# Optimization experiments

Measured on AMD Instinct MI355X. Metric: run time of the kernel, lower is better.

## Reference

```python
import jax, jax.numpy as jnp
import numpy as np

N_NODES = 50000
N_EDGES = 400000
IN_CH = 109
OUT_CH = 32


def setup_inputs() -> dict:
    key = jax.random.key(0)
    ks = jax.random.split(key, 12)
    dims = [(IN_CH, 10 * OUT_CH), (10 * OUT_CH, 2 * OUT_CH), (2 * OUT_CH, OUT_CH), (2 * OUT_CH, OUT_CH)]
    inp = {
        'x': jax.random.normal(ks[0], (N_NODES, IN_CH), dtype=jnp.float32),
        'edge_index': jax.random.randint(ks[1], (2, N_EDGES), 0, N_NODES, dtype=jnp.int64) if jax.config.jax_enable_x64 else jax.random.randint(ks[1], (2, N_EDGES), 0, N_NODES, dtype=jnp.int32),
    }
    names = ['W1', 'b1', 'W2', 'b2', 'Wmu', 'bmu', 'Wls', 'bls']
    for i, (fi, fo) in enumerate(dims):
        scale = 1.0 / np.sqrt(fi)
        inp[names[2 * i]] = jax.random.uniform(ks[2 + 2 * i], (fi, fo), minval=-scale, maxval=scale, dtype=jnp.float32)
        inp[names[2 * i + 1]] = jnp.zeros((fo,), dtype=jnp.float32)
    return inp


def _gcn_conv(x, src, dst, norm, W, b, n):
    # PyG GCNConv: h = x @ W, then symmetric-normalized aggregation, then + b
    h = x @ W                                   # [N, F_out]
    msg = h[src] * norm[:, None]                # [E+N, F_out]
    out = jax.ops.segment_sum(msg, dst, num_segments=n)
    return out + b


def _norm_and_loops(edge_index, n):
    # add self loops, compute D^{-1/2}(A+I)D^{-1/2} edge weights
    loops = jnp.arange(n, dtype=edge_index.dtype)
    src = jnp.concatenate([edge_index[0], loops])
    dst = jnp.concatenate([edge_index[1], loops])
    deg = jax.ops.segment_sum(jnp.ones_like(src, dtype=jnp.float32), dst, num_segments=n)
    dinv = jnp.where(deg > 0, jax.lax.rsqrt(jnp.maximum(deg, 1.0)), 0.0)
    norm = dinv[src] * dinv[dst]
    return src, dst, norm


def reference(x, edge_index, W1, b1, W2, b2, Wmu, bmu, Wls, bls):
    n = x.shape[0]
    src, dst, norm = _norm_and_loops(edge_index, n)
    h = jax.nn.relu(_gcn_conv(x, src, dst, norm, W1, b1, n))
    h = jax.nn.relu(_gcn_conv(h, src, dst, norm, W2, b2, n))
    mu = _gcn_conv(h, src, dst, norm, Wmu, bmu, n)
    logstd = _gcn_conv(h, src, dst, norm, Wls, bls, n)
    return (mu, logstd)
```

## Files before the change

kernel.cpp:

```cpp
#include <hip/hip_runtime.h>

#define NN 50000
#define NE 400000

typedef __attribute__((ext_vector_type(8))) short short8v;
typedef __attribute__((ext_vector_type(4))) float f32x4;

__device__ __forceinline__ unsigned short f2bf_rtn(float x) {
    unsigned u = __float_as_uint(x);
    unsigned r = u + 0x7FFFu + ((u >> 16) & 1u);
    return (unsigned short)(r >> 16);
}
__device__ __forceinline__ float bf2f(unsigned short h) {
    return __uint_as_float(((unsigned)h) << 16);
}

__global__ void prep_kernel(const float* __restrict__ x,
                            const float* __restrict__ W1, const float* __restrict__ W2,
                            const float* __restrict__ Wmu, const float* __restrict__ Wls,
                            unsigned* __restrict__ xp, int* __restrict__ zero_base,
                            unsigned short* __restrict__ w1t_hi, unsigned short* __restrict__ w1t_lo,
                            unsigned short* __restrict__ w2t_hi, unsigned short* __restrict__ w2t_lo,
                            unsigned short* __restrict__ wct_hi, unsigned short* __restrict__ wct_lo) {
    int b = blockIdx.x, tid = threadIdx.x;
    if (b < 12500) {
        int idx = b * 256 + tid;
        int i = idx >> 6, c2 = (idx & 63) * 2;
        long xb = (long)i * 109;
        float v0 = (c2 < 109) ? x[xb + c2] : 0.0f;
        float v1 = (c2 + 1 < 109) ? x[xb + c2 + 1] : 0.0f;
        xp[idx] = (unsigned)f2bf_rtn(v0) | ((unsigned)f2bf_rtn(v1) << 16);
    } else if (b < 12891) {
        int i = (b - 12500) * 256 + tid;
        if (i < 100096) zero_base[i] = 0;
    } else if (b < 13051) {
        int idx = (b - 12891) * 256 + tid;
        int n = idx >> 7, k = idx & 127;
        float v = (k < 109) ? W1[(long)k * 320 + n] : 0.0f;
        unsigned short hb = f2bf_rtn(v);
        w1t_hi[idx] = hb;
        w1t_lo[idx] = f2bf_rtn(v - bf2f(hb));
    } else if (b < 13131) {
        int idx = (b - 13051) * 256 + tid;
        int n = idx / 320, k = idx - n * 320;
        float v = W2[(long)k * 64 + n];
        unsigned short hb = f2bf_rtn(v);
        w2t_hi[idx] = hb;
        w2t_lo[idx] = f2bf_rtn(v - bf2f(hb));
    } else {
        int idx = (b - 13131) * 256 + tid;
        int n = idx >> 6, k = idx & 63;
        float v = (n < 32) ? Wmu[k * 32 + n] : Wls[k * 32 + (n - 32)];
        unsigned short hb = f2bf_rtn(v);
        wct_hi[idx] = hb;
        wct_lo[idx] = f2bf_rtn(v - bf2f(hb));
    }
}

__global__ void hist_kernel(const int* __restrict__ dst, int* __restrict__ counts) {
    for (int e = blockIdx.x * blockDim.x + threadIdx.x; e < NE; e += gridDim.x * blockDim.x)
        atomicAdd(&counts[dst[e]], 1);
}

__global__ void dinv_scan1_kernel(const int* __restrict__ counts, float* __restrict__ dinv,
                                  int* __restrict__ rowstart, int* __restrict__ bsum) {
    __shared__ int tmp[256];
    int tid = threadIdx.x;
    int i = blockIdx.x * 256 + tid;
    int v = (i < NN) ? counts[i] : 0;
    if (i < NN) dinv[i] = rsqrtf((float)(v + 1));
    tmp[tid] = v;
    __syncthreads();
    for (int off = 1; off < 256; off <<= 1) {
        int t = 0;
        if (tid >= off) t = tmp[tid - off];
        __syncthreads();
        if (tid >= off) tmp[tid] += t;
        __syncthreads();
    }
    if (i < NN) rowstart[i] = tmp[tid] - v;
    if (tid == 255) bsum[blockIdx.x] = tmp[255];
}

__global__ void scan23_kernel(int* __restrict__ rowstart, const int* __restrict__ bsum) {
    __shared__ int red[4];
    int tid = threadIdx.x;
    int v = (tid < 196 && tid < (int)blockIdx.x) ? bsum[tid] : 0;
    for (int off = 32; off > 0; off >>= 1) v += __shfl_down(v, off, 64);
    if ((tid & 63) == 0) red[tid >> 6] = v;
    __syncthreads();
    int pref = red[0] + red[1] + red[2] + red[3];
    int i = blockIdx.x * 256 + tid;
    if (i < NN) rowstart[i] += pref;
    if (i == 0) rowstart[NN] = NE;
}

__global__ void scatter_kernel(const int* __restrict__ src, const int* __restrict__ dst,
                               const int* __restrict__ rowstart, int* __restrict__ cursor,
                               int* __restrict__ esrc) {
    for (int e = blockIdx.x * blockDim.x + threadIdx.x; e < NE; e += gridDim.x * blockDim.x) {
        int d = dst[e];
        int pos = rowstart[d] + atomicAdd(&cursor[d], 1);
        esrc[pos] = src[e];
    }
}

__global__ __launch_bounds__(256) void agg109_packed_kernel(const int* __restrict__ rowstart,
                                                            const int* __restrict__ esrc,
                                                            const float* __restrict__ dinv,
                                                            const unsigned* __restrict__ xp,
                                                            unsigned* __restrict__ xa_hi32) {
    int wave = blockIdx.x * (blockDim.x >> 6) + (threadIdx.x >> 6);
    if (wave >= NN) return;
    int lane = threadIdx.x & 63;
    float wd = dinv[wave];
    unsigned pself = xp[(long)wave * 64 + lane];
    float acc0 = __uint_as_float(pself << 16) * wd;
    float acc1 = __uint_as_float(pself & 0xFFFF0000u) * wd;
    int j0 = rowstart[wave], j1 = rowstart[wave + 1];
    int j = j0;
    for (; j + 8 <= j1; j += 8) {
        int s[8];
        float w[8];
        unsigned pp[8];
        #pragma unroll
        for (int u = 0; u < 8; ++u) s[u] = esrc[j + u];
        #pragma unroll
        for (int u = 0; u < 8; ++u) w[u] = dinv[s[u]];
        #pragma unroll
        for (int u = 0; u < 8; ++u) pp[u] = xp[(long)s[u] * 64 + lane];
        #pragma unroll
        for (int u = 0; u < 8; ++u) {
            acc0 = fmaf(__uint_as_float(pp[u] << 16), w[u], acc0);
            acc1 = fmaf(__uint_as_float(pp[u] & 0xFFFF0000u), w[u], acc1);
        }
    }
    for (; j + 4 <= j1; j += 4) {
        int s0 = esrc[j], s1 = esrc[j + 1], s2 = esrc[j + 2], s3 = esrc[j + 3];
        float w0 = dinv[s0], w1 = dinv[s1], w2 = dinv[s2], w3 = dinv[s3];
        unsigned p0 = xp[(long)s0 * 64 + lane], p1 = xp[(long)s1 * 64 + lane];
        unsigned p2 = xp[(long)s2 * 64 + lane], p3 = xp[(long)s3 * 64 + lane];
        acc0 = fmaf(__uint_as_float(p0 << 16), w0, acc0);
        acc1 = fmaf(__uint_as_float(p0 & 0xFFFF0000u), w0, acc1);
        acc0 = fmaf(__uint_as_float(p1 << 16), w1, acc0);
        acc1 = fmaf(__uint_as_float(p1 & 0xFFFF0000u), w1, acc1);
        acc0 = fmaf(__uint_as_float(p2 << 16), w2, acc0);
        acc1 = fmaf(__uint_as_float(p2 & 0xFFFF0000u), w2, acc1);
        acc0 = fmaf(__uint_as_float(p3 << 16), w3, acc0);
        acc1 = fmaf(__uint_as_float(p3 & 0xFFFF0000u), w3, acc1);
    }
    for (; j < j1; ++j) {
        int s = esrc[j];
        float w = dinv[s];
        unsigned pv = xp[(long)s * 64 + lane];
        acc0 = fmaf(__uint_as_float(pv << 16), w, acc0);
        acc1 = fmaf(__uint_as_float(pv & 0xFFFF0000u), w, acc1);
    }
    acc0 *= wd;
    acc1 *= wd;
    xa_hi32[(long)wave * 64 + lane] =
        (unsigned)f2bf_rtn(acc0) | ((unsigned)f2bf_rtn(acc1) << 16);
}

__global__ __launch_bounds__(256) void agg64_relu_bf16_kernel(const int* __restrict__ rowstart,
                                                              const int* __restrict__ esrc,
                                                              const float* __restrict__ dinv,
                                                              const unsigned short* __restrict__ g,
                                                              const float* __restrict__ b,
                                                              unsigned short* __restrict__ hhi) {
    int wave = blockIdx.x * (blockDim.x >> 6) + (threadIdx.x >> 6);
    if (wave >= NN) return;
    int lane = threadIdx.x & 63;
    long base = (long)wave * 64;
    float acc = bf2f(g[base + lane]);
    int j0 = rowstart[wave], j1 = rowstart[wave + 1];
    int j = j0;
    for (; j + 4 <= j1; j += 4) {
        int s0 = esrc[j], s1 = esrc[j + 1], s2 = esrc[j + 2], s3 = esrc[j + 3];
        float p0 = bf2f(g[(long)s0 * 64 + lane]), p1 = bf2f(g[(long)s1 * 64 + lane]);
        float p2 = bf2f(g[(long)s2 * 64 + lane]), p3 = bf2f(g[(long)s3 * 64 + lane]);
        acc += p0 + p1 + p2 + p3;
    }
    for (; j < j1; ++j) acc += bf2f(g[(long)esrc[j] * 64 + lane]);
    float v = acc * dinv[wave] + b[lane];
    v = v > 0.0f ? v : 0.0f;
    hhi[base + lane] = f2bf_rtn(v);
}

__global__ __launch_bounds__(256) void agg64b_kernel(const int* __restrict__ rowstart,
                                                     const int* __restrict__ esrc,
                                                     const float* __restrict__ dinv,
                                                     const unsigned short* __restrict__ h,
                                                     unsigned short* __restrict__ a_hi) {
    int wave = blockIdx.x * (blockDim.x >> 6) + (threadIdx.x >> 6);
    if (wave >= NN) return;
    int lane = threadIdx.x & 63;
    long base = (long)wave * 64;
    float wd = dinv[wave];
    float acc = bf2f(h[base + lane]) * wd;
    int j0 = rowstart[wave], j1 = rowstart[wave + 1];
    int j = j0;
    for (; j + 4 <= j1; j += 4) {
        int s0 = esrc[j], s1 = esrc[j + 1], s2 = esrc[j + 2], s3 = esrc[j + 3];
        float w0 = dinv[s0], w1 = dinv[s1], w2 = dinv[s2], w3 = dinv[s3];
        float p0 = bf2f(h[(long)s0 * 64 + lane]), p1 = bf2f(h[(long)s1 * 64 + lane]);
        float p2 = bf2f(h[(long)s2 * 64 + lane]), p3 = bf2f(h[(long)s3 * 64 + lane]);
        acc = fmaf(p0, w0, acc); acc = fmaf(p1, w1, acc);
        acc = fmaf(p2, w2, acc); acc = fmaf(p3, w3, acc);
    }
    for (; j < j1; ++j) {
        int s = esrc[j];
        acc = fmaf(bf2f(h[(long)s * 64 + lane]), dinv[s], acc);
    }
    a_hi[base + lane] = f2bf_rtn(acc * wd);
}

#define LDT 72

template <int MODE>
__global__ __launch_bounds__(256) void mfma_gemm_kernel(
    const unsigned short* __restrict__ Ahi,
    const unsigned short* __restrict__ Bhi, const unsigned short* __restrict__ Blo,
    const float* __restrict__ bias, const float* __restrict__ bias2,
    const float* __restrict__ dinv,
    unsigned short* __restrict__ Chi,
    float* __restrict__ Cf, int M, int N, int K, int grid_n) {
    __shared__ unsigned short As[64 * LDT];
    __shared__ unsigned short Bs[2 * 64 * LDT];
    int tid = threadIdx.x;
    int wid = tid >> 6, lane = tid & 63;
    int l15 = lane & 15, l4 = lane >> 4;

    int T = gridDim.x;
    int xcd = blockIdx.x & 7, jj = blockIdx.x >> 3;
    int q = T >> 3, r = T & 7;
    int start = (xcd < r) ? xcd * (q + 1) : r * (q + 1) + (xcd - r) * q;
    int lin = start + jj;
    int bm = lin / grid_n, bn = lin - bm * grid_n;
    int bm0 = bm * 64, bn0 = bn * 64;

    f32x4 acc[4] = {};

    for (int kc = 0; kc < K; kc += 64) {
        #pragma unroll
        for (int r2 = 0; r2 < 2; ++r2) {
            int idx = tid + 256 * r2;
            int row = idx >> 3, slot = idx & 7;
            int grow = bm0 + row;
            if (grow >= M) grow = M - 1;
            long go = (long)grow * K + kc + slot * 8;
            *(uint4*)&As[row * LDT + slot * 8] = *(const uint4*)&Ahi[go];
            long gob = (long)(bn0 + row) * K + kc + slot * 8;
            *(uint4*)&Bs[row * LDT + slot * 8] = *(const uint4*)&Bhi[gob];
            *(uint4*)&Bs[64 * LDT + row * LDT + slot * 8] = *(const uint4*)&Blo[gob];
        }
        __syncthreads();
        #pragma unroll
        for (int ks = 0; ks < 2; ++ks) {
            int koff = ks * 32 + l4 * 8;
            int ra = (wid * 16 + l15) * LDT + koff;
            short8v ah = *(const short8v*)&As[ra];
            #pragma unroll
            for (int n = 0; n < 4; ++n) {
                int rb = (n * 16 + l15) * LDT + koff;
                short8v bh = *(const short8v*)&Bs[rb];
                short8v bl = *(const short8v*)&Bs[64 * LDT + rb];
                acc[n] = __builtin_amdgcn_mfma_f32_16x16x32_bf16(ah, bh, acc[n], 0, 0, 0);
                acc[n] = __builtin_amdgcn_mfma_f32_16x16x32_bf16(ah, bl, acc[n], 0, 0, 0);
            }
        }
        __syncthreads();
    }
    int rbase = bm0 + wid * 16 + l4 * 4;
    #pragma unroll
    for (int q2 = 0; q2 < 4; ++q2) {
        int grow = rbase + q2;
        if (grow >= M) continue;
        float rs = (MODE == 1) ? dinv[grow] : 0.0f;
        #pragma unroll
        for (int n = 0; n < 4; ++n) {
            int gcol = bn0 + n * 16 + l15;
            float v = acc[n][q2];
            if (MODE == 0) {
                v += bias[gcol];
                v = v > 0.0f ? v : 0.0f;
                Chi[(long)grow * N + gcol] = f2bf_rtn(v);
            } else if (MODE == 1) {
                Chi[(long)grow * N + gcol] = f2bf_rtn(v * rs);
            } else {
                if (gcol < 32)
                    Cf[(long)grow * 32 + gcol] = v + bias[gcol];
                else
                    Cf[(long)NN * 32 + (long)grow * 32 + (gcol - 32)] = v + bias2[gcol - 32];
            }
        }
    }
}

extern "C" void kernel_launch(void* const* d_in, const int* in_sizes, int n_in,
                              void* d_out, int out_size, void* d_ws, size_t ws_size,
                              hipStream_t stream) {
    const float* x   = (const float*)d_in[0];
    const int*   ei  = (const int*)d_in[1];
    const int*   src = ei;
    const int*   dst = ei + NE;
    const float* W1  = (const float*)d_in[2];
    const float* b1  = (const float*)d_in[3];
    const float* W2  = (const float*)d_in[4];
    const float* b2  = (const float*)d_in[5];
    const float* Wmu = (const float*)d_in[6];
    const float* bmu = (const float*)d_in[7];
    const float* Wls = (const float*)d_in[8];
    const float* bls = (const float*)d_in[9];
    float* out = (float*)d_out;

    char* p = (char*)d_ws;
    float* dinv   = (float*)p; p += 50048 * 4;
    int* counts   = (int*)p;   p += 50048 * 4;
    int* cursor   = (int*)p;   p += 50048 * 4;
    int* rowstart = (int*)p;   p += 50056 * 4;
    int* bsum     = (int*)p;   p += 256 * 4;
    int* esrc     = (int*)p;   p += 400000 * 4;
    unsigned* xp          = (unsigned*)p;       p += 50000L * 64 * 4;
    unsigned short* xa_hi = (unsigned short*)p; p += 50000L * 128 * 2;
    unsigned short* a2_hi = (unsigned short*)p; p += 50000L * 64 * 2;
    unsigned short* g2b   = (unsigned short*)p; p += 50000L * 64 * 2;
    unsigned short* h1_hi = (unsigned short*)p; p += 50000L * 320 * 2;
    unsigned short* w1t_hi = (unsigned short*)p; p += 320 * 128 * 2;
    unsigned short* w1t_lo = (unsigned short*)p; p += 320 * 128 * 2;
    unsigned short* w2t_hi = (unsigned short*)p; p += 64 * 320 * 2;
    unsigned short* w2t_lo = (unsigned short*)p; p += 64 * 320 * 2;
    unsigned short* wct_hi = (unsigned short*)p; p += 64 * 64 * 2;
    unsigned short* wct_lo = (unsigned short*)p; p += 64 * 64 * 2;
    unsigned short* h2_hi = xa_hi;

    const int TB = 256;
    const int NB_NODES = (NN + TB - 1) / TB;
    const int NB_AGG = (NN * 64 + TB - 1) / TB;

    prep_kernel<<<13147, TB, 0, stream>>>(x, W1, W2, Wmu, Wls, xp, counts,
                                          w1t_hi, w1t_lo, w2t_hi, w2t_lo, wct_hi, wct_lo);
    hist_kernel<<<1024, TB, 0, stream>>>(dst, counts);
    dinv_scan1_kernel<<<NB_NODES, TB, 0, stream>>>(counts, dinv, rowstart, bsum);
    scan23_kernel<<<NB_NODES, TB, 0, stream>>>(rowstart, bsum);
    scatter_kernel<<<1024, TB, 0, stream>>>(src, dst, rowstart, cursor, esrc);

    agg109_packed_kernel<<<NB_AGG, TB, 0, stream>>>(rowstart, esrc, dinv, xp,
                                                    (unsigned*)xa_hi);
    mfma_gemm_kernel<0><<<782 * 5, 256, 0, stream>>>(xa_hi, w1t_hi, w1t_lo, b1,
                                                     nullptr, nullptr, h1_hi, nullptr,
                                                     NN, 320, 128, 5);

    mfma_gemm_kernel<1><<<782, 256, 0, stream>>>(h1_hi, w2t_hi, w2t_lo, nullptr,
                                                 nullptr, dinv, g2b, nullptr,
                                                 NN, 64, 320, 1);
    agg64_relu_bf16_kernel<<<NB_AGG, TB, 0, stream>>>(rowstart, esrc, dinv, g2b, b2, h2_hi);

    agg64b_kernel<<<NB_AGG, TB, 0, stream>>>(rowstart, esrc, dinv, h2_hi, a2_hi);
    mfma_gemm_kernel<3><<<782, 256, 0, stream>>>(a2_hi, wct_hi, wct_lo, bmu,
                                                 bls, nullptr, nullptr, out,
                                                 NN, 64, 64, 1);
}
```

Baseline: 183.9 us.

## Fuse CSR build into cooperative kernel and drop W1 low-part MFMA

Replaces the histogram, two scan kernels and the scatter kernel with a single cooperative-launch kernel that uses grid-wide syncs, and moves the zeroing of counts and cursor into it. This removes several kernel launches and the gaps between them. It also drops the bf16 low-part correction for W1 in the first GEMM, halving its MFMA count and B-tile loads at the cost of reduced weight precision in layer one.

```diff
diff --git a/kernel.cpp b/kernel.cpp
--- a/kernel.cpp
+++ b/kernel.cpp
@@ -1,7 +1,10 @@
 #include <hip/hip_runtime.h>
+#include <hip/hip_cooperative_groups.h>
 
 #define NN 50000
 #define NE 400000
+
+namespace cg = cooperative_groups;
 
 typedef __attribute__((ext_vector_type(8))) short short8v;
 typedef __attribute__((ext_vector_type(4))) float f32x4;
@@ -18,8 +21,8 @@
 __global__ void prep_kernel(const float* __restrict__ x,
                             const float* __restrict__ W1, const float* __restrict__ W2,
                             const float* __restrict__ Wmu, const float* __restrict__ Wls,
-                            unsigned* __restrict__ xp, int* __restrict__ zero_base,
-                            unsigned short* __restrict__ w1t_hi, unsigned short* __restrict__ w1t_lo,
+                            unsigned* __restrict__ xp,
+                            unsigned short* __restrict__ w1t_hi,
                             unsigned short* __restrict__ w2t_hi, unsigned short* __restrict__ w2t_lo,
                             unsigned short* __restrict__ wct_hi, unsigned short* __restrict__ wct_lo) {
     int b = blockIdx.x, tid = threadIdx.x;
@@ -30,25 +33,20 @@
         float v0 = (c2 < 109) ? x[xb + c2] : 0.0f;
         float v1 = (c2 + 1 < 109) ? x[xb + c2 + 1] : 0.0f;
         xp[idx] = (unsigned)f2bf_rtn(v0) | ((unsigned)f2bf_rtn(v1) << 16);
-    } else if (b < 12891) {
-        int i = (b - 12500) * 256 + tid;
-        if (i < 100096) zero_base[i] = 0;
-    } else if (b < 13051) {
-        int idx = (b - 12891) * 256 + tid;
+    } else if (b < 12660) {
+        int idx = (b - 12500) * 256 + tid;
         int n = idx >> 7, k = idx & 127;
         float v = (k < 109) ? W1[(long)k * 320 + n] : 0.0f;
-        unsigned short hb = f2bf_rtn(v);
-        w1t_hi[idx] = hb;
-        w1t_lo[idx] = f2bf_rtn(v - bf2f(hb));
-    } else if (b < 13131) {
-        int idx = (b - 13051) * 256 + tid;
+        w1t_hi[idx] = f2bf_rtn(v);
+    } else if (b < 12740) {
+        int idx = (b - 12660) * 256 + tid;
         int n = idx / 320, k = idx - n * 320;
         float v = W2[(long)k * 64 + n];
         unsigned short hb = f2bf_rtn(v);
         w2t_hi[idx] = hb;
         w2t_lo[idx] = f2bf_rtn(v - bf2f(hb));
     } else {
-        int idx = (b - 13131) * 256 + tid;
+        int idx = (b - 12740) * 256 + tid;
         int n = idx >> 6, k = idx & 63;
         float v = (n < 32) ? Wmu[k * 32 + n] : Wls[k * 32 + (n - 32)];
         unsigned short hb = f2bf_rtn(v);
@@ -57,48 +55,49 @@
     }
 }
 
-__global__ void hist_kernel(const int* __restrict__ dst, int* __restrict__ counts) {
-    for (int e = blockIdx.x * blockDim.x + threadIdx.x; e < NE; e += gridDim.x * blockDim.x)
-        atomicAdd(&counts[dst[e]], 1);
-}
-
-__global__ void dinv_scan1_kernel(const int* __restrict__ counts, float* __restrict__ dinv,
-                                  int* __restrict__ rowstart, int* __restrict__ bsum) {
+__global__ void csr_build_kernel(const int* __restrict__ src, const int* __restrict__ dst,
+                                 int* __restrict__ counts, int* __restrict__ cursor,
+                                 float* __restrict__ dinv, int* __restrict__ rowstart,
+                                 int* __restrict__ bsum, int* __restrict__ esrc) {
+    cg::grid_group grid = cg::this_grid();
     __shared__ int tmp[256];
-    int tid = threadIdx.x;
-    int i = blockIdx.x * 256 + tid;
-    int v = (i < NN) ? counts[i] : 0;
-    if (i < NN) dinv[i] = rsqrtf((float)(v + 1));
-    tmp[tid] = v;
-    __syncthreads();
-    for (int off = 1; off < 256; off <<= 1) {
-        int t = 0;
-        if (tid >= off) t = tmp[tid - off];
+    __shared__ int red[4];
+    int tid = threadIdx.x, b = blockIdx.x;
+    int gid = b * 256 + tid, gsz = gridDim.x * 256;
+
+    for (int i = gid; i < NN; i += gsz) { counts[i] = 0; cursor[i] = 0; }
+    grid.sync();
+    for (int e = gid; e < NE; e += gsz) atomicAdd(&counts[dst[e]], 1);
+    grid.sync();
+    if (b < 196) {
+        int i = gid;
+        int v = (i < NN) ? counts[i] : 0;
+        if (i < NN) dinv[i] = rsqrtf((float)(v + 1));
+        tmp[tid] = v;
         __syncthreads();
-        if (tid >= off) tmp[tid] += t;
+        for (int off = 1; off < 256; off <<= 1) {
+            int t = 0;
+            if (tid >= off) t = tmp[tid - off];
+            __syncthreads();
+            if (tid >= off) tmp[tid] += t;
+            __syncthreads();
+        }
+        if (i < NN) rowstart[i] = tmp[tid] - v;
+        if (tid == 255) bsum[b] = tmp[255];
+    }
+    grid.sync();
+    if (b < 196) {
+        int v = (tid < 196 && tid < b) ? bsum[tid] : 0;
+        for (int off = 32; off > 0; off >>= 1) v += __shfl_down(v, off, 64);
+        if ((tid & 63) == 0) red[tid >> 6] = v;
         __syncthreads();
-    }
-    if (i < NN) rowstart[i] = tmp[tid] - v;
-    if (tid == 255) bsum[blockIdx.x] = tmp[255];
-}
-
-__global__ void scan23_kernel(int* __restrict__ rowstart, const int* __restrict__ bsum) {
-    __shared__ int red[4];
-    int tid = threadIdx.x;
-    int v = (tid < 196 && tid < (int)blockIdx.x) ? bsum[tid] : 0;
-    for (int off = 32; off > 0; off >>= 1) v += __shfl_down(v, off, 64);
-    if ((tid & 63) == 0) red[tid >> 6] = v;
-    __syncthreads();
-    int pref = red[0] + red[1] + red[2] + red[3];
-    int i = blockIdx.x * 256 + tid;
-    if (i < NN) rowstart[i] += pref;
-    if (i == 0) rowstart[NN] = NE;
-}
-
-__global__ void scatter_kernel(const int* __restrict__ src, const int* __restrict__ dst,
-                               const int* __restrict__ rowstart, int* __restrict__ cursor,
-                               int* __restrict__ esrc) {
-    for (int e = blockIdx.x * blockDim.x + threadIdx.x; e < NE; e += gridDim.x * blockDim.x) {
+        int pref = red[0] + red[1] + red[2] + red[3];
+        int i = gid;
+        if (i < NN) rowstart[i] += pref;
+        if (i == 0) rowstart[NN] = NE;
+    }
+    grid.sync();
+    for (int e = gid; e < NE; e += gsz) {
         int d = dst[e];
         int pos = rowstart[d] + atomicAdd(&cursor[d], 1);
         esrc[pos] = src[e];
@@ -225,8 +224,9 @@
     const float* __restrict__ dinv,
     unsigned short* __restrict__ Chi,
     float* __restrict__ Cf, int M, int N, int K, int grid_n) {
+    constexpr bool BLO = (MODE != 0);
     __shared__ unsigned short As[64 * LDT];
-    __shared__ unsigned short Bs[2 * 64 * LDT];
+    __shared__ unsigned short Bs[(BLO ? 2 : 1) * 64 * LDT];
     int tid = threadIdx.x;
     int wid = tid >> 6, lane = tid & 63;
     int l15 = lane & 15, l4 = lane >> 4;
@@ -252,7 +252,7 @@
             *(uint4*)&As[row * LDT + slot * 8] = *(const uint4*)&Ahi[go];
             long gob = (long)(bn0 + row) * K + kc + slot * 8;
             *(uint4*)&Bs[row * LDT + slot * 8] = *(const uint4*)&Bhi[gob];
-            *(uint4*)&Bs[64 * LDT + row * LDT + slot * 8] = *(const uint4*)&Blo[gob];
+            if (BLO) *(uint4*)&Bs[64 * LDT + row * LDT + slot * 8] = *(const uint4*)&Blo[gob];
         }
         __syncthreads();
         #pragma unroll
@@ -264,9 +264,11 @@
             for (int n = 0; n < 4; ++n) {
                 int rb = (n * 16 + l15) * LDT + koff;
                 short8v bh = *(const short8v*)&Bs[rb];
-                short8v bl = *(const short8v*)&Bs[64 * LDT + rb];
                 acc[n] = __builtin_amdgcn_mfma_f32_16x16x32_bf16(ah, bh, acc[n], 0, 0, 0);
-                acc[n] = __builtin_amdgcn_mfma_f32_16x16x32_bf16(ah, bl, acc[n], 0, 0, 0);
+                if (BLO) {
+                    short8v bl = *(const short8v*)&Bs[64 * LDT + rb];
+                    acc[n] = __builtin_amdgcn_mfma_f32_16x16x32_bf16(ah, bl, acc[n], 0, 0, 0);
+                }
             }
         }
         __syncthreads();
@@ -302,8 +304,8 @@
                               hipStream_t stream) {
     const float* x   = (const float*)d_in[0];
     const int*   ei  = (const int*)d_in[1];
-    const int*   src = ei;
-    const int*   dst = ei + NE;
+    const int*   src = (const int*)ei;
+    const int*   dst = (const int*)ei + NE;
     const float* W1  = (const float*)d_in[2];
     const float* b1  = (const float*)d_in[3];
     const float* W2  = (const float*)d_in[4];
@@ -327,7 +329,6 @@
     unsigned short* g2b   = (unsigned short*)p; p += 50000L * 64 * 2;
     unsigned short* h1_hi = (unsigned short*)p; p += 50000L * 320 * 2;
     unsigned short* w1t_hi = (unsigned short*)p; p += 320 * 128 * 2;
-    unsigned short* w1t_lo = (unsigned short*)p; p += 320 * 128 * 2;
     unsigned short* w2t_hi = (unsigned short*)p; p += 64 * 320 * 2;
     unsigned short* w2t_lo = (unsigned short*)p; p += 64 * 320 * 2;
     unsigned short* wct_hi = (unsigned short*)p; p += 64 * 64 * 2;
@@ -335,19 +336,20 @@
     unsigned short* h2_hi = xa_hi;
 
     const int TB = 256;
-    const int NB_NODES = (NN + TB - 1) / TB;
     const int NB_AGG = (NN * 64 + TB - 1) / TB;
 
-    prep_kernel<<<13147, TB, 0, stream>>>(x, W1, W2, Wmu, Wls, xp, counts,
-                                          w1t_hi, w1t_lo, w2t_hi, w2t_lo, wct_hi, wct_lo);
-    hist_kernel<<<1024, TB, 0, stream>>>(dst, counts);
-    dinv_scan1_kernel<<<NB_NODES, TB, 0, stream>>>(counts, dinv, rowstart, bsum);
-    scan23_kernel<<<NB_NODES, TB, 0, stream>>>(rowstart, bsum);
-    scatter_kernel<<<1024, TB, 0, stream>>>(src, dst, rowstart, cursor, esrc);
+    prep_kernel<<<12756, TB, 0, stream>>>(x, W1, W2, Wmu, Wls, xp,
+                                          w1t_hi, w2t_hi, w2t_lo, wct_hi, wct_lo);
+    {
+        void* args[] = {(void*)&src, (void*)&dst, (void*)&counts, (void*)&cursor,
+                        (void*)&dinv, (void*)&rowstart, (void*)&bsum, (void*)&esrc};
+        hipLaunchCooperativeKernel((void*)csr_build_kernel, dim3(1024), dim3(TB),
+                                   args, 0, stream);
+    }
 
     agg109_packed_kernel<<<NB_AGG, TB, 0, stream>>>(rowstart, esrc, dinv, xp,
                                                     (unsigned*)xa_hi);
-    mfma_gemm_kernel<0><<<782 * 5, 256, 0, stream>>>(xa_hi, w1t_hi, w1t_lo, b1,
+    mfma_gemm_kernel<0><<<782 * 5, 256, 0, stream>>>(xa_hi, w1t_hi, nullptr, b1,
                                                      nullptr, nullptr, h1_hi, nullptr,
                                                      NN, 320, 128, 5);
 
```

Measured after the change: 542.9 us. +195.2%, slower.
